# Optimization experiments

Measured on AMD Instinct MI355X. Metric: run time of the kernel, lower is better.

The kernel has to match this reference:

```python
import jax, jax.numpy as jnp
import numpy as np


def setup_inputs() -> dict:
    key = jax.random.key(0)
    k1, k2 = jax.random.split(key)
    B, L, D, R = 32, 512, 1024, 128
    batch = jax.random.normal(k1, (B, L, D), dtype=jnp.float32)
    # nn.init.uniform_(proj, -0.05, 0.05)
    proj = jax.random.uniform(k2, (D, R), dtype=jnp.float32, minval=-0.05, maxval=0.05)
    return {"batch": batch, "proj": proj}


def reference(batch, proj):
    # transformed: (B, L, R)
    t = jnp.matmul(batch, proj)
    # Squared L2 all-pairs distance via ||a||^2 + ||b||^2 - 2 a.b
    # (same math as sum((t_i - t_j)^2, -1), avoids the O(B*L*L*R) intermediate)
    sq_norms = jnp.sum(t * t, axis=-1)                      # (B, L)
    cross = jnp.einsum("bir,bjr->bij", t, t)               # (B, L, L)
    d = sq_norms[:, :, None] + sq_norms[:, None, :] - 2.0 * cross
    return jnp.maximum(d, 0.0)  # clamp tiny negative numerical noise
```

## Files before the change

### kernel.cpp

```cpp
#include <hip/hip_runtime.h>
#include <hip/hip_bf16.h>


typedef __attribute__((ext_vector_type(8))) short bf16x8;
typedef __attribute__((ext_vector_type(4))) float f32x4;

typedef __attribute__((address_space(3))) unsigned lds_u;
typedef __attribute__((address_space(1))) const unsigned gbl_u;

__device__ __forceinline__ void async16(void* lds, const void* g) {
    __builtin_amdgcn_global_load_lds((gbl_u*)(unsigned long long)g,
                                     (lds_u*)(unsigned)(unsigned long long)lds,
                                     16, 0, 0);
}

__device__ __forceinline__ unsigned short f2bf(float f) {
    unsigned u = __float_as_uint(f);
    unsigned r = (u + 0x7fffu + ((u >> 16) & 1u)) >> 16;
    return (unsigned short)r;
}
__device__ __forceinline__ float bf2f(unsigned short h) {
    return __uint_as_float(((unsigned)h) << 16);
}
__device__ __forceinline__ bf16x8 pack8(float4 x, float4 y) {
    bf16x8 r;
    r[0] = (short)f2bf(x.x); r[1] = (short)f2bf(x.y);
    r[2] = (short)f2bf(x.z); r[3] = (short)f2bf(x.w);
    r[4] = (short)f2bf(y.x); r[5] = (short)f2bf(y.y);
    r[6] = (short)f2bf(y.z); r[7] = (short)f2bf(y.w);
    return r;
}

__global__ __launch_bounds__(256) void transpose_proj(const float* __restrict__ proj,
                                                      unsigned short* __restrict__ projT) {
    __shared__ unsigned short TsT[128][40];
    const int k0 = blockIdx.x * 32;
    const int t = threadIdx.x;
    const int kl = t >> 3;
    const int seg = t & 7;
    const float* src = proj + (k0 + kl) * 128 + seg * 16;
#pragma unroll
    for (int i = 0; i < 4; ++i) {
        float4 v = *(const float4*)(src + 4 * i);
        int c = seg * 16 + 4 * i;
        TsT[c + 0][kl] = f2bf(v.x);
        TsT[c + 1][kl] = f2bf(v.y);
        TsT[c + 2][kl] = f2bf(v.z);
        TsT[c + 3][kl] = f2bf(v.w);
    }
    __syncthreads();
    const int r = t >> 1, h = t & 1;
#pragma unroll
    for (int i = 0; i < 2; ++i) {
        *(uint4*)(projT + r * 1024 + k0 + h * 16 + 8 * i) =
            *(const uint4*)&TsT[r][h * 16 + 8 * i];
    }
}

__global__ __launch_bounds__(256) void gemm_t(const float* __restrict__ batch,
                                              const unsigned short* __restrict__ projT,
                                              unsigned short* __restrict__ tOut,
                                              float* __restrict__ sqn) {
    __shared__ unsigned char Ls[2][24 * 1024];
    __shared__ float sqpart[2][2][16];

    const int t = threadIdx.x;
    const int wave = t >> 6, lane = t & 63;
    const int wm = wave >> 1, wn = wave & 1;
    const int quad = lane >> 4, l15 = lane & 15;
    const int m0 = blockIdx.x * 32;

    const float* aSrc = batch + (m0 + (wave >> 1) * 16 + l15) * 1024
                      + (wave & 1) * 32 + quad * 8;
    const unsigned short* bSrc[4];
#pragma unroll
    for (int c = 0; c < 4; ++c) {
        int bi = c * 4 + wave;
        bSrc[c] = projT + ((bi >> 3) * 64 + ((bi >> 1) & 3) * 16 + l15) * 1024
                + (bi & 1) * 32 + quad * 8;
    }

    f32x4 acc[4] = {};

    auto stage = [&](int buf, int kk) {
        unsigned char* base = &Ls[buf][0];
        async16(base + (wave * 2 + 0) * 1024 + lane * 16, aSrc + kk);
        async16(base + (wave * 2 + 1) * 1024 + lane * 16, aSrc + kk + 4);
#pragma unroll
        for (int c = 0; c < 4; ++c) {
            int bi = c * 4 + wave;
            async16(base + 8192 + bi * 1024 + lane * 16, bSrc[c] + kk);
        }
    };

    stage(0, 0);
#pragma unroll
    for (int s = 0; s < 16; ++s) {
        __syncthreads();
        if (s < 15) stage((s + 1) & 1, (s + 1) * 64);
        const unsigned char* base = &Ls[s & 1][0];
        bf16x8 af[2];
#pragma unroll
        for (int h = 0; h < 2; ++h) {
            float4 f0 = *(const float4*)(base + ((wm * 2 + h) * 2 + 0) * 1024 + lane * 16);
            float4 f1 = *(const float4*)(base + ((wm * 2 + h) * 2 + 1) * 1024 + lane * 16);
            af[h] = pack8(f0, f1);
        }
#pragma unroll
        for (int fn = 0; fn < 4; ++fn) {
#pragma unroll
            for (int h = 0; h < 2; ++h) {
                int bi = wn * 8 + fn * 2 + h;
                bf16x8 bfr = *(const bf16x8*)(base + 8192 + bi * 1024 + lane * 16);
                acc[fn] = __builtin_amdgcn_mfma_f32_16x16x32_bf16(af[h], bfr, acc[fn], 0, 0, 0);
            }
        }
    }

    float p[4] = {0.f, 0.f, 0.f, 0.f};
#pragma unroll
    for (int fn = 0; fn < 4; ++fn) {
        int col = wn * 64 + fn * 16 + l15;
#pragma unroll
        for (int reg = 0; reg < 4; ++reg) {
            int row = m0 + wm * 16 + quad * 4 + reg;
            unsigned short hb = f2bf(acc[fn][reg]);
            tOut[row * 128 + col] = hb;
            float fv = bf2f(hb);
            p[reg] += fv * fv;
        }
    }
#pragma unroll
    for (int off = 1; off < 16; off <<= 1) {
#pragma unroll
        for (int reg = 0; reg < 4; ++reg) p[reg] += __shfl_xor(p[reg], off);
    }
    if (l15 == 0) {
#pragma unroll
        for (int reg = 0; reg < 4; ++reg) sqpart[wm][wn][quad * 4 + reg] = p[reg];
    }
    __syncthreads();
    if (t < 32) {
        int wmi = t >> 4, ridx = t & 15;
        sqn[m0 + wmi * 16 + ridx] = sqpart[wmi][0][ridx] + sqpart[wmi][1][ridx];
    }
}

__global__ __launch_bounds__(256) void dist_k(const unsigned short* __restrict__ tMat,
                                              const float* __restrict__ sqn,
                                              float* __restrict__ out) {
    __shared__ unsigned char Ls[64 * 1024];

    const int bx = blockIdx.x;
    const int b = bx >> 4, it = (bx >> 2) & 3, jt = bx & 3;
    const int i0 = it * 128, j0 = jt * 128;
    const int t = threadIdx.x;
    const int wave = t >> 6, lane = t & 63;
    const int quad = lane >> 4, l15 = lane & 15;

    const unsigned short* aS = tMat + (b * 512 + j0 + wave * 32 + l15) * 128 + quad * 8;
#pragma unroll
    for (int c = 0; c < 8; ++c)
        async16(&Ls[(wave * 8 + c) * 1024 + lane * 16],
                aS + (c >> 2) * 16 * 128 + (c & 3) * 32);

    const unsigned short* bS = tMat + (b * 512 + i0 + l15) * 128 + quad * 8;
#pragma unroll
    for (int c = 0; c < 8; ++c) {
        int bi = c * 4 + wave;
        async16(&Ls[32768 + bi * 1024 + lane * 16],
                bS + (bi >> 2) * 16 * 128 + (bi & 3) * 32);
    }

    const float* sqb = sqn + b * 512;
    float sqj_[2][4], sqi_[8];
#pragma unroll
    for (int fm = 0; fm < 2; ++fm)
#pragma unroll
        for (int reg = 0; reg < 4; ++reg)
            sqj_[fm][reg] = sqb[j0 + wave * 32 + fm * 16 + quad * 4 + reg];
#pragma unroll
    for (int fn = 0; fn < 8; ++fn)
        sqi_[fn] = sqb[i0 + fn * 16 + l15];

    __syncthreads();

    f32x4 acc[2][8] = {};
#pragma unroll
    for (int ksi = 0; ksi < 4; ++ksi) {
        bf16x8 af[2];
#pragma unroll
        for (int fm = 0; fm < 2; ++fm)
            af[fm] = *(const bf16x8*)&Ls[(wave * 8 + fm * 4 + ksi) * 1024 + lane * 16];
#pragma unroll
        for (int fn = 0; fn < 8; ++fn) {
            bf16x8 bfr = *(const bf16x8*)&Ls[32768 + (fn * 4 + ksi) * 1024 + lane * 16];
#pragma unroll
            for (int fm = 0; fm < 2; ++fm)
                acc[fm][fn] = __builtin_amdgcn_mfma_f32_16x16x32_bf16(af[fm], bfr, acc[fm][fn], 0, 0, 0);
        }
    }

    float* obase = out + (size_t)b * 512 * 512;
#pragma unroll
    for (int fn = 0; fn < 8; ++fn) {
        const int i = i0 + fn * 16 + l15;
        float* orow = obase + (size_t)i * 512 + j0;
        const float si = sqi_[fn];
#pragma unroll
        for (int fm = 0; fm < 2; ++fm) {
            float4 v;
            v.x = fmaxf(si + sqj_[fm][0] - 2.0f * acc[fm][fn][0], 0.0f);
            v.y = fmaxf(si + sqj_[fm][1] - 2.0f * acc[fm][fn][1], 0.0f);
            v.z = fmaxf(si + sqj_[fm][2] - 2.0f * acc[fm][fn][2], 0.0f);
            v.w = fmaxf(si + sqj_[fm][3] - 2.0f * acc[fm][fn][3], 0.0f);
            *(float4*)(orow + wave * 32 + fm * 16 + quad * 4) = v;
        }
    }
}

extern "C" void kernel_launch(void* const* d_in, const int* in_sizes, int n_in,
                              void* d_out, int out_size, void* d_ws, size_t ws_size,
                              hipStream_t stream) {
    (void)in_sizes; (void)n_in; (void)out_size; (void)ws_size;
    const float* batch = (const float*)d_in[0];
    const float* proj  = (const float*)d_in[1];
    float* out = (float*)d_out;

    unsigned short* projT = (unsigned short*)d_ws;
    unsigned short* tMat  = projT + 128 * 1024;
    float* sqn = (float*)(tMat + 16384 * 128);

    hipLaunchKernelGGL(transpose_proj, dim3(32),  dim3(256), 0, stream, proj, projT);
    hipLaunchKernelGGL(gemm_t,         dim3(512), dim3(256), 0, stream, batch, projT, tMat, sqn);
    hipLaunchKernelGGL(dist_k,         dim3(512), dim3(256), 0, stream, tMat, sqn, out);
}
```

Measured before the change: 128.4 us.

## Double gemm_t row tile to 64 rows and specialize waves for A/B loading

Each gemm_t block now computes a 64x128 output tile instead of 32x128, with each wave holding a 32x64 accumulator block, and the grid drops from 512 to 256 blocks. Loading is split by role: waves 0-1 stream the fp32 batch tile and waves 2-3 stream the bf16 projection tile. The goal is to halve redundant reads of the projection matrix and raise MFMA work per staged byte. The trade-off is fewer blocks, roughly one per CU, which may hide memory latency less well in what is largely a bandwidth-bound pass. The squared-norm scratch area now reuses the staging LDS buffer.

```diff
diff --git a/kernel.cpp b/kernel.cpp
--- a/kernel.cpp
+++ b/kernel.cpp
@@ -61,35 +61,44 @@
                                               const unsigned short* __restrict__ projT,
                                               unsigned short* __restrict__ tOut,
                                               float* __restrict__ sqn) {
-    __shared__ unsigned char Ls[2][24 * 1024];
-    __shared__ float sqpart[2][2][16];
+    __shared__ unsigned char Ls[2][32 * 1024];
 
     const int t = threadIdx.x;
     const int wave = t >> 6, lane = t & 63;
     const int wm = wave >> 1, wn = wave & 1;
     const int quad = lane >> 4, l15 = lane & 15;
-    const int m0 = blockIdx.x * 32;
-
-    const float* aSrc = batch + (m0 + (wave >> 1) * 16 + l15) * 1024
-                      + (wave & 1) * 32 + quad * 8;
-    const unsigned short* bSrc[4];
-#pragma unroll
-    for (int c = 0; c < 4; ++c) {
-        int bi = c * 4 + wave;
-        bSrc[c] = projT + ((bi >> 3) * 64 + ((bi >> 1) & 3) * 16 + l15) * 1024
-                + (bi & 1) * 32 + quad * 8;
-    }
-
-    f32x4 acc[4] = {};
+    const int m0 = blockIdx.x * 64;
+
+    f32x4 acc[2][4] = {};
+
+    const float* aS[8];
+    const unsigned short* bS[8];
+    if (wave < 2) {
+#pragma unroll
+        for (int c = 0; c < 8; ++c) {
+            int id = wave * 8 + c;
+            aS[c] = batch + (m0 + (id >> 3) * 32 + ((id >> 2) & 1) * 16 + l15) * 1024
+                  + ((id >> 1) & 1) * 32 + (id & 1) * 4 + quad * 8;
+        }
+    } else {
+#pragma unroll
+        for (int c = 0; c < 8; ++c) {
+            int id = (wave - 2) * 8 + c;
+            bS[c] = projT + ((id >> 3) * 64 + ((id >> 1) & 3) * 16 + l15) * 1024
+                  + (id & 1) * 32 + quad * 8;
+        }
+    }
 
     auto stage = [&](int buf, int kk) {
         unsigned char* base = &Ls[buf][0];
-        async16(base + (wave * 2 + 0) * 1024 + lane * 16, aSrc + kk);
-        async16(base + (wave * 2 + 1) * 1024 + lane * 16, aSrc + kk + 4);
-#pragma unroll
-        for (int c = 0; c < 4; ++c) {
-            int bi = c * 4 + wave;
-            async16(base + 8192 + bi * 1024 + lane * 16, bSrc[c] + kk);
+        if (wave < 2) {
+#pragma unroll
+            for (int c = 0; c < 8; ++c)
+                async16(base + (wave * 8 + c) * 1024 + lane * 16, aS[c] + kk);
+        } else {
+#pragma unroll
+            for (int c = 0; c < 8; ++c)
+                async16(base + 16384 + ((wave - 2) * 8 + c) * 1024 + lane * 16, bS[c] + kk);
         }
     };
 
@@ -99,50 +108,59 @@
         __syncthreads();
         if (s < 15) stage((s + 1) & 1, (s + 1) * 64);
         const unsigned char* base = &Ls[s & 1][0];
-        bf16x8 af[2];
-#pragma unroll
-        for (int h = 0; h < 2; ++h) {
-            float4 f0 = *(const float4*)(base + ((wm * 2 + h) * 2 + 0) * 1024 + lane * 16);
-            float4 f1 = *(const float4*)(base + ((wm * 2 + h) * 2 + 1) * 1024 + lane * 16);
-            af[h] = pack8(f0, f1);
-        }
+        bf16x8 af[2][2];
+#pragma unroll
+        for (int fm = 0; fm < 2; ++fm)
+#pragma unroll
+            for (int h = 0; h < 2; ++h) {
+                float4 f0 = *(const float4*)(base + (wm * 8 + fm * 4 + h * 2 + 0) * 1024 + lane * 16);
+                float4 f1 = *(const float4*)(base + (wm * 8 + fm * 4 + h * 2 + 1) * 1024 + lane * 16);
+                af[fm][h] = pack8(f0, f1);
+            }
+#pragma unroll
+        for (int h = 0; h < 2; ++h)
+#pragma unroll
+            for (int fn = 0; fn < 4; ++fn) {
+                bf16x8 bfr = *(const bf16x8*)(base + 16384 + (wn * 8 + fn * 2 + h) * 1024 + lane * 16);
+#pragma unroll
+                for (int fm = 0; fm < 2; ++fm)
+                    acc[fm][fn] = __builtin_amdgcn_mfma_f32_16x16x32_bf16(af[fm][h], bfr, acc[fm][fn], 0, 0, 0);
+            }
+    }
+
+    float* sqpart = (float*)&Ls[0][0];
+    float p[2][4] = {};
+#pragma unroll
+    for (int fm = 0; fm < 2; ++fm)
 #pragma unroll
         for (int fn = 0; fn < 4; ++fn) {
-#pragma unroll
-            for (int h = 0; h < 2; ++h) {
-                int bi = wn * 8 + fn * 2 + h;
-                bf16x8 bfr = *(const bf16x8*)(base + 8192 + bi * 1024 + lane * 16);
-                acc[fn] = __builtin_amdgcn_mfma_f32_16x16x32_bf16(af[h], bfr, acc[fn], 0, 0, 0);
+            int col = wn * 64 + fn * 16 + l15;
+#pragma unroll
+            for (int reg = 0; reg < 4; ++reg) {
+                int row = m0 + wm * 32 + fm * 16 + quad * 4 + reg;
+                unsigned short hb = f2bf(acc[fm][fn][reg]);
+                tOut[row * 128 + col] = hb;
+                float fv = bf2f(hb);
+                p[fm][reg] += fv * fv;
             }
         }
-    }
-
-    float p[4] = {0.f, 0.f, 0.f, 0.f};
-#pragma unroll
-    for (int fn = 0; fn < 4; ++fn) {
-        int col = wn * 64 + fn * 16 + l15;
-#pragma unroll
-        for (int reg = 0; reg < 4; ++reg) {
-            int row = m0 + wm * 16 + quad * 4 + reg;
-            unsigned short hb = f2bf(acc[fn][reg]);
-            tOut[row * 128 + col] = hb;
-            float fv = bf2f(hb);
-            p[reg] += fv * fv;
-        }
-    }
-#pragma unroll
-    for (int off = 1; off < 16; off <<= 1) {
-#pragma unroll
-        for (int reg = 0; reg < 4; ++reg) p[reg] += __shfl_xor(p[reg], off);
-    }
-    if (l15 == 0) {
-#pragma unroll
-        for (int reg = 0; reg < 4; ++reg) sqpart[wm][wn][quad * 4 + reg] = p[reg];
-    }
+#pragma unroll
+    for (int off = 1; off < 16; off <<= 1)
+#pragma unroll
+        for (int fm = 0; fm < 2; ++fm)
+#pragma unroll
+            for (int reg = 0; reg < 4; ++reg) p[fm][reg] += __shfl_xor(p[fm][reg], off);
+    if (l15 == 0)
+#pragma unroll
+        for (int fm = 0; fm < 2; ++fm)
+#pragma unroll
+            for (int reg = 0; reg < 4; ++reg)
+                sqpart[((wm * 2 + wn) * 2 + fm) * 16 + quad * 4 + reg] = p[fm][reg];
     __syncthreads();
-    if (t < 32) {
-        int wmi = t >> 4, ridx = t & 15;
-        sqn[m0 + wmi * 16 + ridx] = sqpart[wmi][0][ridx] + sqpart[wmi][1][ridx];
+    if (t < 64) {
+        int wmi = t >> 5, rloc = t & 31, fmi = rloc >> 4, r16 = rloc & 15;
+        sqn[m0 + t] = sqpart[((wmi * 2 + 0) * 2 + fmi) * 16 + r16]
+                    + sqpart[((wmi * 2 + 1) * 2 + fmi) * 16 + r16];
     }
 }
 
@@ -232,6 +250,6 @@
     float* sqn = (float*)(tMat + 16384 * 128);
 
     hipLaunchKernelGGL(transpose_proj, dim3(32),  dim3(256), 0, stream, proj, projT);
-    hipLaunchKernelGGL(gemm_t,         dim3(512), dim3(256), 0, stream, batch, projT, tMat, sqn);
+    hipLaunchKernelGGL(gemm_t,         dim3(256), dim3(256), 0, stream, batch, projT, tMat, sqn);
     hipLaunchKernelGGL(dist_k,         dim3(512), dim3(256), 0, stream, tMat, sqn, out);
 }
```

Measured after the change: 133.4 us. +3.9%, slower.

## Load GEMM B operand directly to registers and split distance-kernel K loads

Applied to the files above, without the earlier changes.

In the projection GEMM, the B operand (transposed proj) is now read straight from global memory into registers each K step instead of being staged through LDS. This shrinks the LDS footprint and removes the LDS round trip for B. In the distance kernel, blocks are reordered so the batch index varies fastest. Operand loading is also split into two K halves so the second half's async copies overlap with MFMA work on the first half. The risk is exposed global-load latency for B in the GEMM, plus an extra barrier in the distance kernel.

```diff
diff --git a/kernel.cpp b/kernel.cpp
--- a/kernel.cpp
+++ b/kernel.cpp
@@ -61,7 +61,7 @@
                                               const unsigned short* __restrict__ projT,
                                               unsigned short* __restrict__ tOut,
                                               float* __restrict__ sqn) {
-    __shared__ unsigned char Ls[2][24 * 1024];
+    __shared__ unsigned char Ls[2][8 * 1024];
     __shared__ float sqpart[2][2][16];
 
     const int t = threadIdx.x;
@@ -70,34 +70,35 @@
     const int quad = lane >> 4, l15 = lane & 15;
     const int m0 = blockIdx.x * 32;
 
+    f32x4 acc[4] = {};
+
     const float* aSrc = batch + (m0 + (wave >> 1) * 16 + l15) * 1024
                       + (wave & 1) * 32 + quad * 8;
-    const unsigned short* bSrc[4];
-#pragma unroll
-    for (int c = 0; c < 4; ++c) {
-        int bi = c * 4 + wave;
-        bSrc[c] = projT + ((bi >> 3) * 64 + ((bi >> 1) & 3) * 16 + l15) * 1024
-                + (bi & 1) * 32 + quad * 8;
-    }
-
-    f32x4 acc[4] = {};
-
-    auto stage = [&](int buf, int kk) {
+    const unsigned short* bSrc[4][2];
+#pragma unroll
+    for (int fn = 0; fn < 4; ++fn)
+#pragma unroll
+        for (int h = 0; h < 2; ++h)
+            bSrc[fn][h] = projT + (wn * 64 + fn * 16 + l15) * 1024 + h * 32 + quad * 8;
+
+    auto stageA = [&](int buf, int kk) {
         unsigned char* base = &Ls[buf][0];
         async16(base + (wave * 2 + 0) * 1024 + lane * 16, aSrc + kk);
         async16(base + (wave * 2 + 1) * 1024 + lane * 16, aSrc + kk + 4);
-#pragma unroll
-        for (int c = 0; c < 4; ++c) {
-            int bi = c * 4 + wave;
-            async16(base + 8192 + bi * 1024 + lane * 16, bSrc[c] + kk);
-        }
     };
 
-    stage(0, 0);
+    stageA(0, 0);
 #pragma unroll
     for (int s = 0; s < 16; ++s) {
+        const int kk = s * 64;
+        bf16x8 breg[4][2];
+#pragma unroll
+        for (int fn = 0; fn < 4; ++fn)
+#pragma unroll
+            for (int h = 0; h < 2; ++h)
+                breg[fn][h] = *(const bf16x8*)(bSrc[fn][h] + kk);
         __syncthreads();
-        if (s < 15) stage((s + 1) & 1, (s + 1) * 64);
+        if (s < 15) stageA((s + 1) & 1, kk + 64);
         const unsigned char* base = &Ls[s & 1][0];
         bf16x8 af[2];
 #pragma unroll
@@ -107,14 +108,10 @@
             af[h] = pack8(f0, f1);
         }
 #pragma unroll
-        for (int fn = 0; fn < 4; ++fn) {
-#pragma unroll
-            for (int h = 0; h < 2; ++h) {
-                int bi = wn * 8 + fn * 2 + h;
-                bf16x8 bfr = *(const bf16x8*)(base + 8192 + bi * 1024 + lane * 16);
-                acc[fn] = __builtin_amdgcn_mfma_f32_16x16x32_bf16(af[h], bfr, acc[fn], 0, 0, 0);
-            }
-        }
+        for (int h = 0; h < 2; ++h)
+#pragma unroll
+            for (int fn = 0; fn < 4; ++fn)
+                acc[fn] = __builtin_amdgcn_mfma_f32_16x16x32_bf16(af[h], breg[fn][h], acc[fn], 0, 0, 0);
     }
 
     float p[4] = {0.f, 0.f, 0.f, 0.f};
@@ -152,24 +149,27 @@
     __shared__ unsigned char Ls[64 * 1024];
 
     const int bx = blockIdx.x;
-    const int b = bx >> 4, it = (bx >> 2) & 3, jt = bx & 3;
+    const int b = bx & 31, tile = bx >> 5;
+    const int it = tile >> 2, jt = tile & 3;
     const int i0 = it * 128, j0 = jt * 128;
     const int t = threadIdx.x;
     const int wave = t >> 6, lane = t & 63;
     const int quad = lane >> 4, l15 = lane & 15;
 
     const unsigned short* aS = tMat + (b * 512 + j0 + wave * 32 + l15) * 128 + quad * 8;
-#pragma unroll
-    for (int c = 0; c < 8; ++c)
-        async16(&Ls[(wave * 8 + c) * 1024 + lane * 16],
-                aS + (c >> 2) * 16 * 128 + (c & 3) * 32);
-
     const unsigned short* bS = tMat + (b * 512 + i0 + l15) * 128 + quad * 8;
-#pragma unroll
-    for (int c = 0; c < 8; ++c) {
-        int bi = c * 4 + wave;
-        async16(&Ls[32768 + bi * 1024 + lane * 16],
-                bS + (bi >> 2) * 16 * 128 + (bi & 3) * 32);
+
+#pragma unroll
+    for (int c = 0; c < 4; ++c) {
+        int fm = c >> 1, ksi = c & 1;
+        async16(&Ls[(wave * 8 + fm * 4 + ksi) * 1024 + lane * 16],
+                aS + fm * 16 * 128 + ksi * 32);
+    }
+#pragma unroll
+    for (int c = 0; c < 4; ++c) {
+        int idx = wave * 4 + c, fn = idx >> 1, ksi = idx & 1;
+        async16(&Ls[32768 + (fn * 4 + ksi) * 1024 + lane * 16],
+                bS + fn * 16 * 128 + ksi * 32);
     }
 
     const float* sqb = sqn + b * 512;
@@ -185,9 +185,39 @@
 
     __syncthreads();
 
+#pragma unroll
+    for (int c = 0; c < 4; ++c) {
+        int fm = c >> 1, ksi = 2 + (c & 1);
+        async16(&Ls[(wave * 8 + fm * 4 + ksi) * 1024 + lane * 16],
+                aS + fm * 16 * 128 + ksi * 32);
+    }
+#pragma unroll
+    for (int c = 0; c < 4; ++c) {
+        int idx = wave * 4 + c, fn = idx >> 1, ksi = 2 + (idx & 1);
+        async16(&Ls[32768 + (fn * 4 + ksi) * 1024 + lane * 16],
+                bS + fn * 16 * 128 + ksi * 32);
+    }
+
     f32x4 acc[2][8] = {};
 #pragma unroll
-    for (int ksi = 0; ksi < 4; ++ksi) {
+    for (int ksi = 0; ksi < 2; ++ksi) {
+        bf16x8 af[2];
+#pragma unroll
+        for (int fm = 0; fm < 2; ++fm)
+            af[fm] = *(const bf16x8*)&Ls[(wave * 8 + fm * 4 + ksi) * 1024 + lane * 16];
+#pragma unroll
+        for (int fn = 0; fn < 8; ++fn) {
+            bf16x8 bfr = *(const bf16x8*)&Ls[32768 + (fn * 4 + ksi) * 1024 + lane * 16];
+#pragma unroll
+            for (int fm = 0; fm < 2; ++fm)
+                acc[fm][fn] = __builtin_amdgcn_mfma_f32_16x16x32_bf16(af[fm], bfr, acc[fm][fn], 0, 0, 0);
+        }
+    }
+
+    __syncthreads();
+
+#pragma unroll
+    for (int ksi = 2; ksi < 4; ++ksi) {
         bf16x8 af[2];
 #pragma unroll
         for (int fm = 0; fm < 2; ++fm)
```

After: 137.5 us. 7.0% more time.
